# Kernel tuning notes

Measured on AMD Instinct MI355X. Metric: run time of the kernel, lower is better.

The kernel has to match this reference:

```python
import jax, jax.numpy as jnp
import numpy as np

B, T, D, S = 16, 16384, 256, 4
EPS = 1e-12  # matches torch F.normalize eps


def setup_inputs() -> dict:
    key = jax.random.key(0)
    k1, k2 = jax.random.split(key)
    embeddings = jax.random.normal(k1, (B, T, D), dtype=jnp.float32)
    spk = jax.random.randint(k2, (B, T), 0, S)
    labels = jax.nn.one_hot(spk, S, dtype=jnp.float32)  # [B,T,S] one-hot speaker indicators
    return {"embeddings": embeddings, "labels": labels}


def reference(embeddings, labels):
    # embeddings: [B,T,D], labels: [B,T,S]
    Bv, Tv, _ = embeddings.shape
    # row-wise L2 normalize (torch F.normalize semantics: v / max(||v||, eps))
    n = jnp.linalg.norm(embeddings, axis=-1, keepdims=True)
    V = embeddings / jnp.maximum(n, EPS)
    Y = labels
    # ||V V^T - Y Y^T||_F^2 = ||V^T V||_F^2 - 2||V^T Y||_F^2 + ||Y^T Y||_F^2
    Gvv = jnp.einsum('btd,bte->bde', V, V)   # [B,D,D]
    Gvy = jnp.einsum('btd,bts->bds', V, Y)   # [B,D,S]
    Gyy = jnp.einsum('bts,btu->bsu', Y, Y)   # [B,S,S]
    sq = lambda g: jnp.sum(g * g, axis=(1, 2))
    per_b = (sq(Gvv) - 2.0 * sq(Gvy) + sq(Gyy)) / (Tv * Tv)  # [B]
    return jnp.mean(per_b)
```

## Files before the change

### kernel.cpp

```cpp
#include <hip/hip_runtime.h>

#define NB 16
#define NT 16384
#define ND 256
#define NS 4
#define SLICES 16
#define TPB 1024
#define CHUNK 32
#define NITER (TPB / CHUNK)

typedef float          f32x4 __attribute__((ext_vector_type(4)));
typedef short          s16x8 __attribute__((ext_vector_type(8)));
typedef unsigned short u16x4 __attribute__((ext_vector_type(4)));

__device__ __forceinline__ unsigned short f2bf(float f) {
  unsigned int u = __float_as_uint(f);
  return (unsigned short)((u + 0x7FFFu + ((u >> 16) & 1u)) >> 16);
}

__global__ __launch_bounds__(1024) void fused_gram(
    const float* __restrict__ emb, const float* __restrict__ lab,
    float* __restrict__ P, float* __restrict__ PY, float* __restrict__ CntP)
{
  const int tid  = threadIdx.x;
  const int lane = tid & 63;
  const int w    = tid >> 6;
  const int b     = blockIdx.x >> 4;
  const int slice = blockIdx.x & 15;
  const int t0    = slice * TPB;

  __shared__ __align__(16) unsigned short rm[CHUNK * ND];
  __shared__ __align__(16) unsigned short blkT[4 * ND * 8];
  __shared__ unsigned int spk2[TPB / 16];
  __shared__ float cnt_l[NS];

  if (tid < TPB / 16) spk2[tid] = 0u;
  if (tid < NS) cnt_l[tid] = 0.0f;
  __syncthreads();

  {
    f32x4 y = ((const f32x4*)(lab + ((size_t)b * NT + t0) * NS))[tid];
    int s = (int)(y.y + 2.0f * y.z + 3.0f * y.w + 0.5f);
    atomicOr(&spk2[tid >> 4], (unsigned)s << (2 * (tid & 15)));
    unsigned long long m0 = __ballot(s == 0);
    unsigned long long m1 = __ballot(s == 1);
    unsigned long long m2 = __ballot(s == 2);
    unsigned long long m3 = __ballot(s == 3);
    if (lane == 0) {
      atomicAdd(&cnt_l[0], (float)__popcll(m0));
      atomicAdd(&cnt_l[1], (float)__popcll(m1));
      atomicAdd(&cnt_l[2], (float)__popcll(m2));
      atomicAdd(&cnt_l[3], (float)__popcll(m3));
    }
  }

  const float* embB = emb + ((size_t)b * NT + t0) * ND;
  const int r = w >> 2, c = w & 3;

  f32x4 acc[4][4];
  f32x4 yacc = (f32x4){0.f, 0.f, 0.f, 0.f};
  #pragma unroll
  for (int i = 0; i < 4; ++i)
    #pragma unroll
    for (int j = 0; j < 4; ++j) acc[i][j] = (f32x4){0.f, 0.f, 0.f, 0.f};

  f32x4 pf[2];
  #pragma unroll
  for (int j = 0; j < 2; ++j)
    pf[j] = *(const f32x4*)(embB + (size_t)(2 * w + j) * ND + 4 * lane);

  __syncthreads();

  const int quad = lane >> 4, m16 = lane & 15;

  for (int it = 0; it < NITER; ++it) {
    #pragma unroll
    for (int j = 0; j < 2; ++j) {
      f32x4 v = pf[j];
      float ss = v.x * v.x + v.y * v.y + v.z * v.z + v.w * v.w;
      #pragma unroll
      for (int off = 32; off; off >>= 1) ss += __shfl_xor(ss, off);
      float sc = 1.0f / fmaxf(sqrtf(ss), 1e-12f);
      u16x4 st;
      st.x = f2bf(v.x * sc); st.y = f2bf(v.y * sc);
      st.z = f2bf(v.z * sc); st.w = f2bf(v.w * sc);
      *(u16x4*)&rm[(2 * w + j) * ND + 4 * lane] = st;
    }
    if (it + 1 < NITER) {
      const float* p = embB + (size_t)((it + 1) * CHUNK + 2 * w) * ND + 4 * lane;
      #pragma unroll
      for (int j = 0; j < 2; ++j) pf[j] = *(const f32x4*)(p + j * ND);
    }
    __syncthreads();

    {
      int tg = tid >> 8, d = tid & 255;
      s16x8 v8;
      #pragma unroll
      for (int s8 = 0; s8 < 8; ++s8)
        v8[s8] = (short)rm[(tg * 8 + s8) * ND + d];
      *(s16x8*)&blkT[(tg * ND + d) * 8] = v8;
    }
    __syncthreads();

    {
      const short* bp = (const short*)blkT;
      s16x8 afr[4];
      #pragma unroll
      for (int mi = 0; mi < 4; ++mi)
        afr[mi] = *(const s16x8*)(bp + ((quad * ND + (4 * r + mi) * 16 + m16) << 3));

      {
        unsigned sw = spk2[it * 2 + (quad >> 1)];
        s16x8 y8;
        #pragma unroll
        for (int j = 0; j < 8; ++j) {
          int sp = (int)((sw >> (2 * ((quad & 1) * 8 + j))) & 3u);
          y8[j] = (sp == m16) ? (short)0x3F80 : (short)0;
        }
        yacc = __builtin_amdgcn_mfma_f32_16x16x32_bf16(afr[c], y8, yacc, 0, 0, 0);
      }

      #pragma unroll
      for (int nj = 0; nj < 4; ++nj) {
        s16x8 bfr = *(const s16x8*)(bp + ((quad * ND + (4 * c + nj) * 16 + m16) << 3));
        #pragma unroll
        for (int mi = 0; mi < 4; ++mi)
          acc[mi][nj] = __builtin_amdgcn_mfma_f32_16x16x32_bf16(afr[mi], bfr, acc[mi][nj], 0, 0, 0);
      }
    }
  }

  {
    float* Pb = P + ((size_t)blockIdx.x << 16);
    #pragma unroll
    for (int mi = 0; mi < 4; ++mi)
      #pragma unroll
      for (int nj = 0; nj < 4; ++nj)
        #pragma unroll
        for (int rr = 0; rr < 4; ++rr) {
          int row = r * 64 + mi * 16 + quad * 4 + rr;
          int col = c * 64 + nj * 16 + m16;
          Pb[row * ND + col] = acc[mi][nj][rr];
        }
    float* PYb = PY + ((size_t)blockIdx.x << 12);
    #pragma unroll
    for (int rr = 0; rr < 4; ++rr)
      PYb[(w * 16 + quad * 4 + rr) * 16 + m16] = yacc[rr];
    if (tid < NS) CntP[blockIdx.x * NS + tid] = cnt_l[tid];
  }
}

__global__ __launch_bounds__(256) void finalize_kernel(
    const float* __restrict__ P, const float* __restrict__ PY,
    const float* __restrict__ CntP, float* __restrict__ out)
{
  const int b = blockIdx.x >> 4, seg = blockIdx.x & 15;
  const int tid = threadIdx.x;
  float local = 0.f;

  const float* Pb = P + ((size_t)b * 16) * 65536 + seg * 4096;
  #pragma unroll 4
  for (int k = 0; k < 16; ++k) {
    int e = tid + k * 256;
    float g = 0.f;
    #pragma unroll
    for (int s = 0; s < 16; ++s) g += Pb[(size_t)s * 65536 + e];
    local = fmaf(g, g, local);
  }
  if (seg == 0) {
    const float* Yb = PY + ((size_t)b * 16) * 4096;
    #pragma unroll 4
    for (int k = 0; k < 16; ++k) {
      int e = tid + k * 256;
      float g = 0.f;
      #pragma unroll
      for (int s = 0; s < 16; ++s) g += Yb[(size_t)s * 4096 + e];
      local = fmaf(-2.f * g, g, local);
    }
    if (tid < NS) {
      float ct = 0.f;
      for (int s = 0; s < 16; ++s) ct += CntP[(b * 16 + s) * NS + tid];
      local = fmaf(ct, ct, local);
    }
  }
  #pragma unroll
  for (int off = 32; off; off >>= 1) local += __shfl_xor(local, off);
  __shared__ float wsum[4];
  if ((tid & 63) == 0) wsum[tid >> 6] = local;
  __syncthreads();
  if (tid == 0) {
    float s = wsum[0] + wsum[1] + wsum[2] + wsum[3];
    atomicAdd(out, s * (1.0f / 4294967296.0f));
  }
}

extern "C" void kernel_launch(void* const* d_in, const int* in_sizes, int n_in,
                              void* d_out, int out_size, void* d_ws, size_t ws_size,
                              hipStream_t stream) {
  const float* emb = (const float*)d_in[0];
  const float* lab = (const float*)d_in[1];
  float* out = (float*)d_out;

  float* P    = (float*)d_ws;
  float* PY   = P + (size_t)256 * 65536;
  float* CntP = PY + (size_t)256 * 4096;

  hipMemsetAsync(d_out, 0, sizeof(float), stream);

  fused_gram<<<dim3(NB * SLICES), dim3(1024), 0, stream>>>(emb, lab, P, PY, CntP);
  finalize_kernel<<<dim3(NB * SLICES), dim3(256), 0, stream>>>(P, PY, CntP, out);
}
```

Measured before the change: 474.3 us.

## Write normalized rows directly in MFMA-transposed layout with larger chunks and fewer barriers

Each wave now normalizes 8 rows and writes them straight into the k-major packed bf16 layout the MFMA reads, which removes the intermediate row-major LDS buffer and the separate transpose pass. The chunk grows from 32 to 128 rows, so each loop iteration issues four k-steps of MFMAs. Speaker one-hot fragments are precomputed once into LDS instead of being rebuilt every iteration. The two __syncthreads per step become raw s_barrier instructions with manual lgkmcnt waits, which cuts synchronization. In exchange it uses more LDS and registers per thread, and correctness now depends on the hand-placed barriers.

```diff
diff --git a/kernel.cpp b/kernel.cpp
--- a/kernel.cpp
+++ b/kernel.cpp
@@ -6,17 +6,19 @@
 #define NS 4
 #define SLICES 16
 #define TPB 1024
-#define CHUNK 32
+#define CHUNK 128
 #define NITER (TPB / CHUNK)
 
-typedef float          f32x4 __attribute__((ext_vector_type(4)));
-typedef short          s16x8 __attribute__((ext_vector_type(8)));
-typedef unsigned short u16x4 __attribute__((ext_vector_type(4)));
+typedef float f32x4 __attribute__((ext_vector_type(4)));
+typedef short s16x8 __attribute__((ext_vector_type(8)));
 
 __device__ __forceinline__ unsigned short f2bf(float f) {
   unsigned int u = __float_as_uint(f);
   return (unsigned short)((u + 0x7FFFu + ((u >> 16) & 1u)) >> 16);
 }
+
+#define BAR_LGKM() asm volatile("s_waitcnt lgkmcnt(0)\n\ts_barrier" ::: "memory")
+#define BAR_RAW()  asm volatile("s_barrier" ::: "memory")
 
 __global__ __launch_bounds__(1024) void fused_gram(
     const float* __restrict__ emb, const float* __restrict__ lab,
@@ -27,19 +29,27 @@
   const int w    = tid >> 6;
   const int b     = blockIdx.x >> 4;
   const int slice = blockIdx.x & 15;
-  const int t0    = slice * TPB;
-
-  __shared__ __align__(16) unsigned short rm[CHUNK * ND];
-  __shared__ __align__(16) unsigned short blkT[4 * ND * 8];
-  __shared__ unsigned int spk2[TPB / 16];
+
+  __shared__ __align__(16) unsigned short blkT[4 * 4 * ND * 8];
+  __shared__ __align__(16) unsigned short Yf[32 * 64 * 8];
+  __shared__ unsigned int spk2[64];
   __shared__ float cnt_l[NS];
 
-  if (tid < TPB / 16) spk2[tid] = 0u;
+  if (tid < 64) spk2[tid] = 0u;
   if (tid < NS) cnt_l[tid] = 0.0f;
+
+  const float* embB  = emb + ((size_t)b * NT + slice * TPB) * ND;
+  const float* wbase = embB + (size_t)(w * 8) * ND + 4 * lane;
+
+  f32x4 pf[4];
+  #pragma unroll
+  for (int j = 0; j < 4; ++j)
+    pf[j] = *(const f32x4*)(wbase + (size_t)j * ND);
+
   __syncthreads();
 
   {
-    f32x4 y = ((const f32x4*)(lab + ((size_t)b * NT + t0) * NS))[tid];
+    f32x4 y = ((const f32x4*)(lab + ((size_t)b * NT + slice * TPB) * NS))[tid];
     int s = (int)(y.y + 2.0f * y.z + 3.0f * y.w + 0.5f);
     atomicOr(&spk2[tid >> 4], (unsigned)s << (2 * (tid & 15)));
     unsigned long long m0 = __ballot(s == 0);
@@ -53,9 +63,27 @@
       atomicAdd(&cnt_l[3], (float)__popcll(m3));
     }
   }
-
-  const float* embB = emb + ((size_t)b * NT + t0) * ND;
+  __syncthreads();
+
+  #pragma unroll
+  for (int rr2 = 0; rr2 < 2; ++rr2) {
+    int rho  = tid * 2 + rr2;
+    int step = rho >> 6, ln = rho & 63;
+    int q = ln >> 4, col = ln & 15;
+    unsigned wv = spk2[step * 2 + (q >> 1)];
+    int base = (q & 1) * 16;
+    s16x8 y8;
+    #pragma unroll
+    for (int j = 0; j < 8; ++j) {
+      int sp = (int)((wv >> (base + 2 * j)) & 3u);
+      y8[j] = (sp == col) ? (short)0x3F80 : (short)0;
+    }
+    ((s16x8*)Yf)[rho] = y8;
+  }
+  __syncthreads();
+
   const int r = w >> 2, c = w & 3;
+  const int quad = lane >> 4, m16 = lane & 15;
 
   f32x4 acc[4][4];
   f32x4 yacc = (f32x4){0.f, 0.f, 0.f, 0.f};
@@ -64,71 +92,67 @@
     #pragma unroll
     for (int j = 0; j < 4; ++j) acc[i][j] = (f32x4){0.f, 0.f, 0.f, 0.f};
 
-  f32x4 pf[2];
-  #pragma unroll
-  for (int j = 0; j < 2; ++j)
-    pf[j] = *(const f32x4*)(embB + (size_t)(2 * w + j) * ND + 4 * lane);
-
-  __syncthreads();
-
-  const int quad = lane >> 4, m16 = lane & 15;
+  const s16x8* bp = (const s16x8*)blkT;
+  const s16x8* yp = (const s16x8*)Yf;
+  s16x8* wp = (s16x8*)blkT;
 
   for (int it = 0; it < NITER; ++it) {
-    #pragma unroll
-    for (int j = 0; j < 2; ++j) {
-      f32x4 v = pf[j];
-      float ss = v.x * v.x + v.y * v.y + v.z * v.z + v.w * v.w;
+    const float* ib = wbase + (size_t)it * CHUNK * ND;
+
+    f32x4 vb[4];
+    #pragma unroll
+    for (int j = 0; j < 4; ++j)
+      vb[j] = *(const f32x4*)(ib + (size_t)(4 + j) * ND);
+
+    unsigned short sv[8][4];
+    #pragma unroll
+    for (int j = 0; j < 8; ++j) {
+      f32x4 v = (j < 4) ? pf[j] : vb[j - 4];
+      float ss = fmaf(v.x, v.x, fmaf(v.y, v.y, fmaf(v.z, v.z, v.w * v.w)));
       #pragma unroll
       for (int off = 32; off; off >>= 1) ss += __shfl_xor(ss, off);
       float sc = 1.0f / fmaxf(sqrtf(ss), 1e-12f);
-      u16x4 st;
-      st.x = f2bf(v.x * sc); st.y = f2bf(v.y * sc);
-      st.z = f2bf(v.z * sc); st.w = f2bf(v.w * sc);
-      *(u16x4*)&rm[(2 * w + j) * ND + 4 * lane] = st;
-    }
+      sv[j][0] = f2bf(v.x * sc); sv[j][1] = f2bf(v.y * sc);
+      sv[j][2] = f2bf(v.z * sc); sv[j][3] = f2bf(v.w * sc);
+    }
+    #pragma unroll
+    for (int q = 0; q < 4; ++q) {
+      s16x8 row;
+      #pragma unroll
+      for (int j = 0; j < 8; ++j) row[j] = (short)sv[j][q];
+      wp[w * ND + 4 * lane + q] = row;
+    }
+
     if (it + 1 < NITER) {
-      const float* p = embB + (size_t)((it + 1) * CHUNK + 2 * w) * ND + 4 * lane;
-      #pragma unroll
-      for (int j = 0; j < 2; ++j) pf[j] = *(const f32x4*)(p + j * ND);
-    }
-    __syncthreads();
-
-    {
-      int tg = tid >> 8, d = tid & 255;
-      s16x8 v8;
-      #pragma unroll
-      for (int s8 = 0; s8 < 8; ++s8)
-        v8[s8] = (short)rm[(tg * 8 + s8) * ND + d];
-      *(s16x8*)&blkT[(tg * ND + d) * 8] = v8;
-    }
-    __syncthreads();
-
-    {
-      const short* bp = (const short*)blkT;
+      const float* nb = wbase + (size_t)(it + 1) * CHUNK * ND;
+      #pragma unroll
+      for (int j = 0; j < 4; ++j)
+        pf[j] = *(const f32x4*)(nb + (size_t)j * ND);
+    }
+
+    BAR_LGKM();
+
+    #pragma unroll
+    for (int kk = 0; kk < 4; ++kk) {
+      const int kb = (kk * 4 + quad) * ND;
       s16x8 afr[4];
       #pragma unroll
       for (int mi = 0; mi < 4; ++mi)
-        afr[mi] = *(const s16x8*)(bp + ((quad * ND + (4 * r + mi) * 16 + m16) << 3));
-
-      {
-        unsigned sw = spk2[it * 2 + (quad >> 1)];
-        s16x8 y8;
-        #pragma unroll
-        for (int j = 0; j < 8; ++j) {
-          int sp = (int)((sw >> (2 * ((quad & 1) * 8 + j))) & 3u);
-          y8[j] = (sp == m16) ? (short)0x3F80 : (short)0;
-        }
-        yacc = __builtin_amdgcn_mfma_f32_16x16x32_bf16(afr[c], y8, yacc, 0, 0, 0);
-      }
+        afr[mi] = bp[kb + r * 64 + mi * 16 + m16];
+
+      s16x8 yfr = yp[(it * 4 + kk) * 64 + lane];
+      yacc = __builtin_amdgcn_mfma_f32_16x16x32_bf16(afr[c], yfr, yacc, 0, 0, 0);
 
       #pragma unroll
       for (int nj = 0; nj < 4; ++nj) {
-        s16x8 bfr = *(const s16x8*)(bp + ((quad * ND + (4 * c + nj) * 16 + m16) << 3));
+        s16x8 bfr = bp[kb + c * 64 + nj * 16 + m16];
         #pragma unroll
         for (int mi = 0; mi < 4; ++mi)
           acc[mi][nj] = __builtin_amdgcn_mfma_f32_16x16x32_bf16(afr[mi], bfr, acc[mi][nj], 0, 0, 0);
       }
     }
+
+    BAR_RAW();
   }
 
   {
```

Result: slower. 588.7 us (+24.1%).
